# Kernel tuning notes

Hardware: AMD Instinct MI355X
Metric: run time of the kernel (lower is better)

Reference implementation:

```python
import jax, jax.numpy as jnp
import numpy as np

N_EMBD = 1024
N_HEAD = 16
DIM_HEAD = N_EMBD // N_HEAD
# Source code divides scores by scale = dim_head**-0.5, i.e. multiplies by sqrt(dim_head).
INV_SCALE = 1.0 / (DIM_HEAD ** -0.5)


def setup_inputs() -> dict:
    key = jax.random.key(0)
    k1, k2, k3 = jax.random.split(key, 3)
    x = jax.random.normal(k1, (4, 2048, N_EMBD), dtype=jnp.float32)
    # Linear(n_embd, 3*n_embd, bias=False): y = x @ W_qkv  (W stored as [C, 3C])
    W_qkv = jax.random.normal(k2, (N_EMBD, 3 * N_EMBD), dtype=jnp.float32) * (N_EMBD ** -0.5)
    W_proj = jax.random.normal(k3, (N_EMBD, N_EMBD), dtype=jnp.float32) * (N_EMBD ** -0.5)
    return {"x": x, "W_qkv": W_qkv, "W_proj": W_proj}


def reference(x, W_qkv, W_proj):
    B, T, C = x.shape
    qkv = jnp.einsum('btc,cd->btd', x, W_qkv)  # [B,T,3C]
    q, k, v = jnp.split(qkv, 3, axis=-1)
    # [B,T,C] -> [B,H,T,Dh]
    def to_heads(t):
        return t.reshape(B, T, N_HEAD, DIM_HEAD).transpose(0, 2, 1, 3)
    q, k, v = to_heads(q), to_heads(k), to_heads(v)
    scores = jnp.einsum('bhqd,bhkd->bhqk', q, k) * INV_SCALE  # faithful to /scale bug
    causal = jnp.tril(jnp.ones((T, T), dtype=bool))
    scores = jnp.where(causal[None, None], scores, -jnp.inf)
    attn = jax.nn.softmax(scores, axis=-1)
    y = jnp.einsum('bhqk,bhkd->bhqd', attn, v)  # [B,H,T,Dh]
    y = y.transpose(0, 2, 1, 3).reshape(B, T, C)
    return jnp.einsum('btc,cd->btd', y, W_proj)
```

## Files before the change

kernel.cpp:

```cpp
#include <hip/hip_runtime.h>
#include <stdint.h>

typedef unsigned short ushort_t;
typedef __attribute__((ext_vector_type(8))) short short8;
typedef __attribute__((ext_vector_type(8))) _Float16 half8;
typedef __attribute__((ext_vector_type(4))) float f32x4;
typedef __attribute__((ext_vector_type(4))) unsigned short us4;

#define AS1 __attribute__((address_space(1)))
#define AS3 __attribute__((address_space(3)))

#if __has_builtin(__builtin_amdgcn_exp2f)
#define EXP2(x) __builtin_amdgcn_exp2f(x)
#else
#define EXP2(x) exp2f(x)
#endif

#define SC 11.541560327111707f

__device__ __forceinline__ ushort_t f2h(float f) {
  _Float16 h = (_Float16)f;
  return __builtin_bit_cast(unsigned short, h);
}

__device__ __forceinline__ void gload16(const void* g, void* l) {
  __builtin_amdgcn_global_load_lds((AS1 const void*)g, (AS3 void*)l, 16, 0, 0);
}

__device__ __forceinline__ f32x4 mfma16(short8 a, short8 b, f32x4 c) {
  return __builtin_amdgcn_mfma_f32_16x16x32_f16(
      __builtin_bit_cast(half8, a), __builtin_bit_cast(half8, b), c, 0, 0, 0);
}

__global__ __launch_bounds__(256) void cast_f32_f16(const float4* __restrict__ in,
                                                    us4* __restrict__ out, int n4) {
  int i = blockIdx.x * 256 + threadIdx.x;
  int stride = gridDim.x * 256;
  for (; i < n4; i += stride) {
    float4 v = in[i];
    us4 o;
    o[0] = f2h(v.x); o[1] = f2h(v.y); o[2] = f2h(v.z); o[3] = f2h(v.w);
    out[i] = o;
  }
}

__global__ __launch_bounds__(256) void tcast(const float* __restrict__ in,
                                             ushort_t* __restrict__ out, int R, int C) {
  __shared__ __align__(16) float lt[32][33];
  const int r0 = blockIdx.y * 32, c0 = blockIdx.x * 32;
  const int i = threadIdx.x;
  const int lr = i >> 3, lc = (i & 7) * 4;
  float4 v = *(const float4*)(in + (size_t)(r0 + lr) * C + c0 + lc);
  lt[lr][lc + 0] = v.x; lt[lr][lc + 1] = v.y; lt[lr][lc + 2] = v.z; lt[lr][lc + 3] = v.w;
  __syncthreads();
  const int oc = i >> 3;
  const int orr = (i & 7) * 4;
  us4 o;
#pragma unroll
  for (int jj = 0; jj < 4; ++jj) o[jj] = f2h(lt[orr + jj][oc]);
  *(us4*)(out + (size_t)(c0 + oc) * R + r0 + orr) = o;
}

template<int MODE>
__global__ __launch_bounds__(256) void gemm128(
    const ushort_t* __restrict__ A, const ushort_t* __restrict__ Bt, int K, int N,
    ushort_t* __restrict__ qo, ushort_t* __restrict__ ko, ushort_t* __restrict__ vo,
    float* __restrict__ outp)
{
  __shared__ __align__(16) unsigned char lds[32768];
  const int tid = threadIdx.x;
  const int lane = tid & 63, w = tid >> 6;
  const int ln = lane & 15, gq = lane >> 4;
  const int wr = w >> 1, wc = w & 1;
  const int m0 = blockIdx.y * 128, n0 = blockIdx.x * 128;
  const size_t ldb = (size_t)K * 2;
  const unsigned char* ab = (const unsigned char*)A + (size_t)m0 * ldb;
  const unsigned char* bb = (const unsigned char*)Bt + (size_t)n0 * ldb;
  f32x4 acc[4][4] = {};
  const int nkt = K >> 6;
  for (int kb = 0; kb < nkt; ++kb) {
    const unsigned char* abk = ab + kb * 128;
    const unsigned char* bbk = bb + kb * 128;
#pragma unroll
    for (int e = 0; e < 4; ++e) {
      unsigned o = e * 4096 + tid * 16;
      unsigned r = o >> 7;
      unsigned c = (o & 127) ^ ((r & 7) << 4);
      gload16(abk + (size_t)r * ldb + c, lds + o);
      gload16(bbk + (size_t)r * ldb + c, lds + 16384 + o);
    }
    __syncthreads();
    short8 af[4][2], bf8[4][2];
#pragma unroll
    for (int mi = 0; mi < 4; ++mi) {
      unsigned row = wr * 64 + mi * 16 + ln;
      unsigned c0 = (gq * 16) ^ ((row & 7) << 4);
      af[mi][0] = *(const short8*)(lds + row * 128 + c0);
      af[mi][1] = *(const short8*)(lds + row * 128 + (c0 ^ 64));
    }
#pragma unroll
    for (int ni = 0; ni < 4; ++ni) {
      unsigned row = wc * 64 + ni * 16 + ln;
      unsigned c0 = (gq * 16) ^ ((row & 7) << 4);
      bf8[ni][0] = *(const short8*)(lds + 16384 + row * 128 + c0);
      bf8[ni][1] = *(const short8*)(lds + 16384 + row * 128 + (c0 ^ 64));
    }
#pragma unroll
    for (int mi = 0; mi < 4; ++mi)
#pragma unroll
      for (int ni = 0; ni < 4; ++ni) {
        acc[mi][ni] = mfma16(af[mi][0], bf8[ni][0], acc[mi][ni]);
        acc[mi][ni] = mfma16(af[mi][1], bf8[ni][1], acc[mi][ni]);
      }
    __syncthreads();
  }
  if (MODE == 0) {
#pragma unroll
    for (int mi = 0; mi < 4; ++mi)
#pragma unroll
      for (int ni = 0; ni < 4; ++ni)
#pragma unroll
        for (int j = 0; j < 4; ++j) {
          int token = m0 + wr * 64 + mi * 16 + gq * 4 + j;
          int feat  = n0 + wc * 64 + ni * 16 + ln;
          int sec = feat >> 10, cc = feat & 1023;
          int hh = cc >> 6, dd = cc & 63;
          size_t off = (((size_t)(token >> 11) * 16 + hh) * 2048 + (token & 2047)) * 64 + dd;
          ushort_t valb = f2h(acc[mi][ni][j]);
          if (sec == 0) qo[off] = valb;
          else if (sec == 1) ko[off] = valb;
          else vo[off] = valb;
        }
  } else {
#pragma unroll
    for (int mi = 0; mi < 4; ++mi)
#pragma unroll
      for (int ni = 0; ni < 4; ++ni)
#pragma unroll
        for (int j = 0; j < 4; ++j) {
          int token = m0 + wr * 64 + mi * 16 + gq * 4 + j;
          int feat  = n0 + wc * 64 + ni * 16 + ln;
          outp[(size_t)token * N + feat] = acc[mi][ni][j];
        }
  }
}

__global__ __launch_bounds__(256) void transpose_v(const ushort_t* __restrict__ vn,
                                                   ushort_t* __restrict__ vt) {
  __shared__ __align__(16) ushort_t lt[64][80];
  const int bh = blockIdx.y, t0 = blockIdx.x * 64;
  const int i = threadIdx.x;
  {
    const int tr = i >> 2, dc = (i & 3) * 16;
    const ushort_t* src = vn + ((size_t)bh * 2048 + t0 + tr) * 64 + dc;
    *(short8*)&lt[tr][dc] = *(const short8*)src;
    *(short8*)&lt[tr][dc + 8] = *(const short8*)(src + 8);
  }
  __syncthreads();
  {
    const int dr = i >> 2, tc = (i & 3) * 16;
    short8 a, b;
#pragma unroll
    for (int jj = 0; jj < 8; ++jj) a[jj] = (short)lt[tc + jj][dr];
#pragma unroll
    for (int jj = 0; jj < 8; ++jj) b[jj] = (short)lt[tc + 8 + jj][dr];
    ushort_t* dst = vt + ((size_t)bh * 64 + dr) * 2048 + t0 + tc;
    *(short8*)dst = a;
    *(short8*)(dst + 8) = b;
  }
}

__global__ __launch_bounds__(256) void attn_kernel(const ushort_t* __restrict__ qg,
                                                   const ushort_t* __restrict__ kg,
                                                   const ushort_t* __restrict__ vtg,
                                                   ushort_t* __restrict__ yg) {
  __shared__ __align__(16) unsigned char lds[40960];
  const int n = blockIdx.x;
  const int xcd = n & 7, loc = n >> 3;
  const int bh = xcd * 8 + (loc >> 4);
  const int pair = loc & 15;
  const int tid = threadIdx.x;
  const int lane = tid & 63, w = tid >> 6;
  const int ln = lane & 15, gq = lane >> 4;

  const unsigned char* kbase = (const unsigned char*)kg + (size_t)bh * 2048 * 128;
  const unsigned char* vbase = (const unsigned char*)vtg + (size_t)bh * 64 * 4096;
  const ushort_t* qg_bh = qg + (size_t)bh * 2048 * 64;
  const unsigned pw = 32768 + w * 2048;

  auto stage = [&](int buf, int t) {
    const unsigned char* kt = kbase + (size_t)t * 8192;
    const unsigned char* vt = vbase + t * 128;
#pragma unroll
    for (int e = 0; e < 2; ++e) {
      unsigned o = e * 4096 + tid * 16;
      unsigned r = o >> 7;
      unsigned c = (o & 127) ^ ((r & 7) << 4);
      gload16(kt + r * 128 + c, lds + buf * 8192 + o);
      gload16(vt + (size_t)r * 4096 + c, lds + 16384 + buf * 8192 + o);
    }
  };

  int cur = 0;
  for (int ph = 0; ph < 2; ++ph) {
    const int qt = (ph == 0) ? pair : 31 - pair;
    const int q0 = qt * 64;
    const int nt = qt + 1;

    const ushort_t* qrow = qg_bh + (size_t)(q0 + w * 16 + ln) * 64;
    short8 qa0 = *(const short8*)(qrow + gq * 8);
    short8 qa1 = *(const short8*)(qrow + 32 + gq * 8);

    f32x4 yacc[4] = {};
    float mrow = -3e38f, lrow = 0.f;

    stage(cur, 0);
    __syncthreads();

    for (int t = 0; t < nt; ++t) {
      if (t + 1 < nt) stage(cur ^ 1, t + 1);
      const unsigned kb_ = cur * 8192;
      const unsigned vb_ = 16384 + cur * 8192;
      f32x4 s[4];
#pragma unroll
      for (int f = 0; f < 4; ++f) {
        unsigned row = f * 16 + ln;
        unsigned c0 = (gq * 16) ^ ((row & 7) << 4);
        short8 k0 = *(const short8*)(lds + kb_ + row * 128 + c0);
        short8 k1 = *(const short8*)(lds + kb_ + row * 128 + (c0 ^ 64));
        f32x4 z = {0.f, 0.f, 0.f, 0.f};
        z = mfma16(k0, qa0, z);
        s[f] = mfma16(k1, qa1, z);
      }
      if (t == nt - 1) {
        int qloc = w * 16 + ln;
#pragma unroll
        for (int f = 0; f < 4; ++f) {
          int kvb = f * 16 + gq * 4;
#pragma unroll
          for (int j = 0; j < 4; ++j)
            if (kvb + j > qloc) s[f][j] = -3e38f;
        }
      }
      {
        float rm = s[0][0];
#pragma unroll
        for (int f = 0; f < 4; ++f)
#pragma unroll
          for (int j = 0; j < 4; ++j) rm = fmaxf(rm, s[f][j]);
        rm = fmaxf(rm, __shfl_xor(rm, 16));
        rm = fmaxf(rm, __shfl_xor(rm, 32));
        float mnew = fmaxf(mrow, rm);
        float alpha = EXP2((mrow - mnew) * SC);
        float rs = 0.f;
#pragma unroll
        for (int f = 0; f < 4; ++f)
#pragma unroll
          for (int j = 0; j < 4; ++j) {
            float p = EXP2((s[f][j] - mnew) * SC);
            s[f][j] = p;
            rs += p;
          }
        rs += __shfl_xor(rs, 16);
        rs += __shfl_xor(rs, 32);
        lrow = lrow * alpha + rs;
        mrow = mnew;
#pragma unroll
        for (int j = 0; j < 4; ++j) {
          float aj = __shfl(alpha, gq * 4 + j);
#pragma unroll
          for (int df = 0; df < 4; ++df) yacc[df][j] *= aj;
        }
      }
#pragma unroll
      for (int f = 0; f < 4; ++f) {
        us4 pk;
#pragma unroll
        for (int j = 0; j < 4; ++j) pk[j] = f2h(s[f][j]);
        unsigned addr = (pw + ln * 128 + (f * 16 + gq * 4) * 2) ^ ((ln & 7) << 4);
        *(us4*)(lds + addr) = pk;
      }
#pragma unroll
      for (int st = 0; st < 2; ++st) {
        unsigned pc = (st * 64 + gq * 16) ^ ((ln & 7) << 4);
        short8 pa = *(const short8*)(lds + pw + ln * 128 + pc);
#pragma unroll
        for (int df = 0; df < 4; ++df) {
          unsigned row = df * 16 + ln;
          unsigned c0 = (st * 64 + gq * 16) ^ ((row & 7) << 4);
          short8 vb = *(const short8*)(lds + vb_ + row * 128 + c0);
          yacc[df] = mfma16(pa, vb, yacc[df]);
        }
      }
      __syncthreads();
      cur ^= 1;
    }

#pragma unroll
    for (int j = 0; j < 4; ++j) {
      float lj = __shfl(lrow, gq * 4 + j);
      float rl = 1.0f / lj;
      int tq = q0 + w * 16 + gq * 4 + j;
#pragma unroll
      for (int df = 0; df < 4; ++df) {
        int col = (bh & 15) * 64 + df * 16 + ln;
        size_t off = ((size_t)(bh >> 4) * 2048 + tq) * 1024 + col;
        yg[off] = f2h(yacc[df][j] * rl);
      }
    }
  }
}

extern "C" void kernel_launch(void* const* d_in, const int* in_sizes, int n_in,
                              void* d_out, int out_size, void* d_ws, size_t ws_size,
                              hipStream_t stream) {
  (void)in_sizes; (void)n_in; (void)out_size; (void)ws_size;
  const float* x     = (const float*)d_in[0];
  const float* wqkv  = (const float*)d_in[1];
  const float* wproj = (const float*)d_in[2];
  float* out = (float*)d_out;
  char* ws = (char*)d_ws;
  ushort_t* xb   = (ushort_t*)(ws);
  ushort_t* wqkt = (ushort_t*)(ws + 16777216);
  ushort_t* wpt  = (ushort_t*)(ws + 23068672);
  ushort_t* qb_  = (ushort_t*)(ws + 25165824);
  ushort_t* kb_  = (ushort_t*)(ws + 41943040);
  ushort_t* vn   = (ushort_t*)(ws + 58720256);
  ushort_t* vt   = (ushort_t*)(ws + 75497472);
  ushort_t* yb   = xb;

  cast_f32_f16<<<2048, 256, 0, stream>>>((const float4*)x, (us4*)xb, 2097152);
  tcast<<<dim3(96, 32), 256, 0, stream>>>(wqkv, wqkt, 1024, 3072);
  tcast<<<dim3(32, 32), 256, 0, stream>>>(wproj, wpt, 1024, 1024);
  gemm128<0><<<dim3(24, 64), 256, 0, stream>>>(xb, wqkt, 1024, 3072, qb_, kb_, vn, nullptr);
  transpose_v<<<dim3(32, 64), 256, 0, stream>>>(vn, vt);
  attn_kernel<<<1024, 256, 0, stream>>>(qb_, kb_, vt, yb);
  gemm128<1><<<dim3(8, 64), 256, 0, stream>>>(yb, wpt, 1024, 1024, nullptr, nullptr, nullptr, out);
}
```

Before: 197.0 us.

## Fuse V transpose into QKV GEMM epilogue, add lazy softmax rescale and setprio

The QKV GEMM epilogue now writes V directly in transposed [bh, d, t] layout using 4-wide packed stores, which removes the separate transpose_v kernel launch and its extra read and write of V. The attention kernel skips the online-softmax rescale unless some row's max grows by more than a threshold, and folds the scale into an FMA before exp2. It also raises wave priority around the MFMA blocks. The lazy rescale lets exponent arguments run above zero by a bounded amount, which is safe in fp32 but adds some numerical risk.

After: 186.7 us. -5.2%, faster.

```diff
diff --git a/kernel.cpp b/kernel.cpp
--- a/kernel.cpp
+++ b/kernel.cpp
@@ -118,19 +118,27 @@
 #pragma unroll
     for (int mi = 0; mi < 4; ++mi)
 #pragma unroll
-      for (int ni = 0; ni < 4; ++ni)
-#pragma unroll
-        for (int j = 0; j < 4; ++j) {
-          int token = m0 + wr * 64 + mi * 16 + gq * 4 + j;
-          int feat  = n0 + wc * 64 + ni * 16 + ln;
-          int sec = feat >> 10, cc = feat & 1023;
-          int hh = cc >> 6, dd = cc & 63;
-          size_t off = (((size_t)(token >> 11) * 16 + hh) * 2048 + (token & 2047)) * 64 + dd;
-          ushort_t valb = f2h(acc[mi][ni][j]);
-          if (sec == 0) qo[off] = valb;
-          else if (sec == 1) ko[off] = valb;
-          else vo[off] = valb;
-        }
+      for (int ni = 0; ni < 4; ++ni) {
+        int feat = n0 + wc * 64 + ni * 16 + ln;
+        int sec = feat >> 10, cc = feat & 1023;
+        int hh = cc >> 6, dd = cc & 63;
+        int tokbase = m0 + wr * 64 + mi * 16 + gq * 4;
+        int bh = (tokbase >> 11) * 16 + hh;
+        int tloc = tokbase & 2047;
+        if (sec == 2) {
+          us4 pk;
+#pragma unroll
+          for (int j = 0; j < 4; ++j) pk[j] = f2h(acc[mi][ni][j]);
+          *(us4*)(vo + ((size_t)bh * 64 + dd) * 2048 + tloc) = pk;
+        } else {
+          ushort_t* dst = (sec == 0) ? qo : ko;
+#pragma unroll
+          for (int j = 0; j < 4; ++j) {
+            size_t off = ((size_t)bh * 2048 + tloc + j) * 64 + dd;
+            dst[off] = f2h(acc[mi][ni][j]);
+          }
+        }
+      }
   } else {
 #pragma unroll
     for (int mi = 0; mi < 4; ++mi)
@@ -142,31 +150,6 @@
           int feat  = n0 + wc * 64 + ni * 16 + ln;
           outp[(size_t)token * N + feat] = acc[mi][ni][j];
         }
-  }
-}
-
-__global__ __launch_bounds__(256) void transpose_v(const ushort_t* __restrict__ vn,
-                                                   ushort_t* __restrict__ vt) {
-  __shared__ __align__(16) ushort_t lt[64][80];
-  const int bh = blockIdx.y, t0 = blockIdx.x * 64;
-  const int i = threadIdx.x;
-  {
-    const int tr = i >> 2, dc = (i & 3) * 16;
-    const ushort_t* src = vn + ((size_t)bh * 2048 + t0 + tr) * 64 + dc;
-    *(short8*)&lt[tr][dc] = *(const short8*)src;
-    *(short8*)&lt[tr][dc + 8] = *(const short8*)(src + 8);
-  }
-  __syncthreads();
-  {
-    const int dr = i >> 2, tc = (i & 3) * 16;
-    short8 a, b;
-#pragma unroll
-    for (int jj = 0; jj < 8; ++jj) a[jj] = (short)lt[tc + jj][dr];
-#pragma unroll
-    for (int jj = 0; jj < 8; ++jj) b[jj] = (short)lt[tc + 8 + jj][dr];
-    ushort_t* dst = vt + ((size_t)bh * 64 + dr) * 2048 + t0 + tc;
-    *(short8*)dst = a;
-    *(short8*)(dst + 8) = b;
   }
 }
 
@@ -222,6 +205,7 @@
       const unsigned kb_ = cur * 8192;
       const unsigned vb_ = 16384 + cur * 8192;
       f32x4 s[4];
+      __builtin_amdgcn_s_setprio(1);
 #pragma unroll
       for (int f = 0; f < 4; ++f) {
         unsigned row = f * 16 + ln;
@@ -232,6 +216,7 @@
         z = mfma16(k0, qa0, z);
         s[f] = mfma16(k1, qa1, z);
       }
+      __builtin_amdgcn_s_setprio(0);
       if (t == nt - 1) {
         int qloc = w * 16 + ln;
 #pragma unroll
@@ -250,27 +235,31 @@
           for (int j = 0; j < 4; ++j) rm = fmaxf(rm, s[f][j]);
         rm = fmaxf(rm, __shfl_xor(rm, 16));
         rm = fmaxf(rm, __shfl_xor(rm, 32));
-        float mnew = fmaxf(mrow, rm);
-        float alpha = EXP2((mrow - mnew) * SC);
+        if (__any((rm - mrow) * SC > 8.0f)) {
+          float mnew = fmaxf(mrow, rm);
+          float alpha = EXP2((mrow - mnew) * SC);
+          lrow *= alpha;
+          mrow = mnew;
+#pragma unroll
+          for (int j = 0; j < 4; ++j) {
+            float aj = __shfl(alpha, gq * 4 + j);
+#pragma unroll
+            for (int df = 0; df < 4; ++df) yacc[df][j] *= aj;
+          }
+        }
+        float msc = mrow * SC;
         float rs = 0.f;
 #pragma unroll
         for (int f = 0; f < 4; ++f)
 #pragma unroll
           for (int j = 0; j < 4; ++j) {
-            float p = EXP2((s[f][j] - mnew) * SC);
+            float p = EXP2(__builtin_fmaf(s[f][j], SC, -msc));
             s[f][j] = p;
             rs += p;
           }
         rs += __shfl_xor(rs, 16);
         rs += __shfl_xor(rs, 32);
-        lrow = lrow * alpha + rs;
-        mrow = mnew;
-#pragma unroll
-        for (int j = 0; j < 4; ++j) {
-          float aj = __shfl(alpha, gq * 4 + j);
-#pragma unroll
-          for (int df = 0; df < 4; ++df) yacc[df][j] *= aj;
-        }
+        lrow += rs;
       }
 #pragma unroll
       for (int f = 0; f < 4; ++f) {
@@ -280,6 +269,7 @@
         unsigned addr = (pw + ln * 128 + (f * 16 + gq * 4) * 2) ^ ((ln & 7) << 4);
         *(us4*)(lds + addr) = pk;
       }
+      __builtin_amdgcn_s_setprio(1);
 #pragma unroll
       for (int st = 0; st < 2; ++st) {
         unsigned pc = (st * 64 + gq * 16) ^ ((ln & 7) << 4);
@@ -292,6 +282,7 @@
           yacc[df] = mfma16(pa, vb, yacc[df]);
         }
       }
+      __builtin_amdgcn_s_setprio(0);
       __syncthreads();
       cur ^= 1;
     }
@@ -325,15 +316,13 @@
   ushort_t* wpt  = (ushort_t*)(ws + 23068672);
   ushort_t* qb_  = (ushort_t*)(ws + 25165824);
   ushort_t* kb_  = (ushort_t*)(ws + 41943040);
-  ushort_t* vn   = (ushort_t*)(ws + 58720256);
   ushort_t* vt   = (ushort_t*)(ws + 75497472);
   ushort_t* yb   = xb;
 
   cast_f32_f16<<<2048, 256, 0, stream>>>((const float4*)x, (us4*)xb, 2097152);
   tcast<<<dim3(96, 32), 256, 0, stream>>>(wqkv, wqkt, 1024, 3072);
   tcast<<<dim3(32, 32), 256, 0, stream>>>(wproj, wpt, 1024, 1024);
-  gemm128<0><<<dim3(24, 64), 256, 0, stream>>>(xb, wqkt, 1024, 3072, qb_, kb_, vn, nullptr);
-  transpose_v<<<dim3(32, 64), 256, 0, stream>>>(vn, vt);
+  gemm128<0><<<dim3(24, 64), 256, 0, stream>>>(xb, wqkt, 1024, 3072, qb_, kb_, vt, nullptr);
   attn_kernel<<<1024, 256, 0, stream>>>(qb_, kb_, vt, yb);
   gemm128<1><<<dim3(8, 64), 256, 0, stream>>>(yb, wpt, 1024, 1024, nullptr, nullptr, nullptr, out);
 }
```
